# Optimization experiments

Measured on AMD Instinct MI355X. Metric: run time of the kernel, lower is better.

The kernel has to match this reference:

```python
import jax, jax.numpy as jnp
import numpy as np

EMB = 512
HEADS = 8


def setup_inputs() -> dict:
    key = jax.random.key(0)
    ks = jax.random.split(key, 5)
    B, N, E = 4, 2048, EMB
    x = jax.random.normal(ks[0], (B, N, E), dtype=jnp.float32)
    # Linear weights stored [in, out] so y = x @ W + b (matches torch x @ W.T + b with W.T)
    W_qkv = jax.random.normal(ks[1], (E, 3 * E), dtype=jnp.float32) * (E ** -0.5)
    b_qkv = jax.random.normal(ks[2], (3 * E,), dtype=jnp.float32) * 0.02
    W_proj = jax.random.normal(ks[3], (E, E), dtype=jnp.float32) * (E ** -0.5)
    b_proj = jax.random.normal(ks[4], (E,), dtype=jnp.float32) * 0.02
    return {"x": x, "W_qkv": W_qkv, "b_qkv": b_qkv, "W_proj": W_proj, "b_proj": b_proj}


def reference(x, W_qkv, b_qkv, W_proj, b_proj):
    B, N, E = x.shape
    H = HEADS
    D = E // H
    qkv = x @ W_qkv + b_qkv                      # [B, N, 3E]
    # einops 'b n (h d qkv) -> qkv b h n d': last dim splits as (h, d, 3) -> q/k/v interleaved
    qkv = qkv.reshape(B, N, H, D, 3)
    q = jnp.transpose(qkv[..., 0], (0, 2, 1, 3))  # [B, H, N, D]
    k = jnp.transpose(qkv[..., 1], (0, 2, 1, 3))
    v = jnp.transpose(qkv[..., 2], (0, 2, 1, 3))
    scale = jnp.asarray(E, x.dtype) ** 0.5        # divides by sqrt(emb_size), as in source
    energies = jnp.einsum('bhqd,bhkd->bhqk', q, k) / scale
    attention = jax.nn.softmax(energies, axis=-1)
    out = jnp.einsum('bhqk,bhkd->bhqd', attention, v)
    out = jnp.transpose(out, (0, 2, 1, 3)).reshape(B, N, E)
    return out @ W_proj + b_proj
```

## Files before the change

### kernel.cpp

```cpp
#include <hip/hip_runtime.h>
#include <hip/hip_bf16.h>

typedef __hip_bfloat16 bf16;
typedef __attribute__((ext_vector_type(8))) short short8;
typedef __attribute__((ext_vector_type(4))) float f32x4;
typedef __attribute__((ext_vector_type(16))) float f32x16;

static constexpr float QSCALE = 1.4426950408889634f / 22.627416997969522f;

__device__ __forceinline__ void gload_lds16(const void* g, void* l) {
  __builtin_amdgcn_global_load_lds((const __attribute__((address_space(1))) unsigned*)(g),
                                   (__attribute__((address_space(3))) unsigned*)(l), 16, 0, 0);
}

__device__ __forceinline__ unsigned cvtpk(float a, float b) {
  unsigned r;
  asm("v_cvt_pk_bf16_f32 %0, %1, %2" : "=v"(r) : "v"(a), "v"(b));
  return r;
}

__global__ __launch_bounds__(256) void cvt_x_kernel(const float* __restrict__ x,
                                                    bf16* __restrict__ xb, int n8) {
  for (int i = blockIdx.x * 256 + threadIdx.x; i < n8; i += gridDim.x * 256) {
    const float4* src = (const float4*)(x) + (size_t)i * 2;
    float4 a = src[0], b = src[1];
    union { short8 v; unsigned u[4]; } o;
    o.u[0] = cvtpk(a.x, a.y);
    o.u[1] = cvtpk(a.z, a.w);
    o.u[2] = cvtpk(b.x, b.y);
    o.u[3] = cvtpk(b.z, b.w);
    *(short8*)(xb + (size_t)i * 8) = o.v;
  }
}

__global__ __launch_bounds__(256) void transpose_cvt(const float* __restrict__ W,
                                                     bf16* __restrict__ Wt,
                                                     int Nout, int permute) {
  __shared__ float tile[64][65];
  const int j0 = blockIdx.x * 64, k0 = blockIdx.y * 64;
  const int tx = threadIdx.x & 63, ty = threadIdx.x >> 6;
  for (int r = ty; r < 64; r += 4)
    tile[r][tx] = W[(size_t)(k0 + r) * Nout + j0 + tx];
  __syncthreads();
  for (int r = ty; r < 64; r += 4) {
    int j = j0 + r;
    int jp = j;
    if (permute) {
      int h = j / 192, rr = j % 192, d = rr / 3, s = rr % 3;
      jp = s * 512 + h * 64 + d;
    }
    Wt[(size_t)jp * 512 + k0 + tx] = __float2bfloat16(tile[tx][r]);
  }
}

template <int MODE>
__global__ __launch_bounds__(256) void gemm_bt(const bf16* __restrict__ A,
                                               const bf16* __restrict__ Bt,
                                               const float* __restrict__ bias,
                                               bf16* __restrict__ Qb, bf16* __restrict__ Kb,
                                               bf16* __restrict__ Vt,
                                               float* __restrict__ Cout) {
  __shared__ short Alds[128 * 32];
  __shared__ short Blds[128 * 32];
  const int t = threadIdx.x;
  const int w = t >> 6;
  const int wr = w >> 1, wc = w & 1;
  const int lr = t & 15;
  const int lq = (t >> 4) & 3;
  const int bm = blockIdx.x, bn = blockIdx.y;

  f32x4 acc[4][4];
#pragma unroll
  for (int m = 0; m < 4; ++m)
#pragma unroll
    for (int n = 0; n < 4; ++n)
#pragma unroll
      for (int j = 0; j < 4; ++j) acc[m][n][j] = 0.f;

  for (int kt = 0; kt < 16; ++kt) {
#pragma unroll
    for (int i = 0; i < 2; ++i) {
      const int c = i * 256 + t;
      gload_lds16(A + (size_t)(bm * 128 + (c >> 2)) * 512 + kt * 32 + (c & 3) * 8,
                  &Alds[(i * 256 + w * 64) * 8]);
      gload_lds16(Bt + (size_t)(bn * 128 + (c >> 2)) * 512 + kt * 32 + (c & 3) * 8,
                  &Blds[(i * 256 + w * 64) * 8]);
    }
    __syncthreads();
    short8 af[4], bfr[4];
#pragma unroll
    for (int m = 0; m < 4; ++m)
      af[m] = *(const short8*)&Alds[(wr * 64 + m * 16 + lr) * 32 + lq * 8];
#pragma unroll
    for (int n = 0; n < 4; ++n)
      bfr[n] = *(const short8*)&Blds[(wc * 64 + n * 16 + lr) * 32 + lq * 8];
#pragma unroll
    for (int m = 0; m < 4; ++m)
#pragma unroll
      for (int n = 0; n < 4; ++n)
        acc[m][n] = __builtin_amdgcn_mfma_f32_16x16x32_bf16(af[m], bfr[n], acc[m][n], 0, 0, 0);
    __syncthreads();
  }

#pragma unroll
  for (int m = 0; m < 4; ++m) {
#pragma unroll
    for (int n = 0; n < 4; ++n) {
      const int col = bn * 128 + wc * 64 + n * 16 + lr;
#pragma unroll
      for (int j = 0; j < 4; ++j) {
        const int row = bm * 128 + wr * 64 + m * 16 + lq * 4 + j;
        float v = acc[m][n][j];
        if (MODE == 0) {
          const int s = col >> 9, h = (col >> 6) & 7, d = col & 63;
          v += bias[h * 192 + d * 3 + s];
          const int hd = col & 511;
          if (s == 0)
            Qb[(size_t)row * 512 + hd] = __float2bfloat16(v * QSCALE);
          else if (s == 1)
            Kb[(size_t)row * 512 + hd] = __float2bfloat16(v);
          else
            Vt[((size_t)((row >> 11) * 8 + h) * 64 + d) * 2048 + (row & 2047)] =
                __float2bfloat16(v);
        } else {
          v += bias[col];
          Cout[(size_t)row * 512 + col] = v;
        }
      }
    }
  }
}

__global__ __launch_bounds__(128) void attn_fwd(const bf16* __restrict__ Q,
                                                const bf16* __restrict__ K,
                                                const bf16* __restrict__ Vt,
                                                bf16* __restrict__ O) {
  __shared__ short Klds[2][64 * 64];
  __shared__ short Vlds[2][64 * 64];
  const int t = threadIdx.x;
  const int w = t >> 6;
  const int l = t & 63;
  const int lo = l & 31;
  const int hi = l >> 5;
  const int bid = blockIdx.x;
  const int bh = bid & 31, qt = bid >> 5;
  const int b = bh >> 3, h = bh & 7;
  const int qg = qt * 64 + w * 32 + lo;

  const bf16* Kb = K + (size_t)b * 2048 * 512 + h * 64;
  const bf16* Vb = Vt + (size_t)bh * 64 * 2048;

  const bf16* qptr = Q + ((size_t)b * 2048 + qg) * 512 + h * 64 + hi * 8;
  short8 qf[4];
#pragma unroll
  for (int kk = 0; kk < 4; ++kk) qf[kk] = *(const short8*)(qptr + kk * 16);

  union { unsigned u[4]; short8 v; } ones;
#pragma unroll
  for (int j = 0; j < 4; ++j) ones.u[j] = 0x3F803F80u;

  f32x16 zv;
#pragma unroll
  for (int r = 0; r < 16; ++r) zv[r] = 0.f;

  f32x16 acc0, acc1, ssum;
#pragma unroll
  for (int r = 0; r < 16; ++r) { acc0[r] = 0.f; acc1[r] = 0.f; ssum[r] = 0.f; }

#define STAGE(BUF, KV0)                                                              \
  do {                                                                               \
    _Pragma("unroll") for (int i = 0; i < 4; ++i) {                                  \
      const int c = i * 128 + t, r = c >> 3, g = (c & 7) ^ (r & 7);                  \
      gload_lds16(Kb + (size_t)((KV0) + r) * 512 + g * 8,                            \
                  &Klds[BUF][(i * 128 + w * 64) * 8]);                               \
    }                                                                                \
    _Pragma("unroll") for (int i = 0; i < 4; ++i) {                                  \
      const int c = i * 128 + t, r = c >> 3, g = (c & 7) ^ (r & 7);                  \
      gload_lds16(Vb + (size_t)r * 2048 + (KV0) + g * 8,                             \
                  &Vlds[BUF][(i * 128 + w * 64) * 8]);                               \
    }                                                                                \
  } while (0)

  STAGE(0, 0);
  __syncthreads();

  int buf = 0;
  for (int it = 0; it < 32; ++it) {
    if (it + 1 < 32) STAGE(buf ^ 1, (it + 1) * 64);

    const char* kl = (const char*)&Klds[buf][0];
    const char* vl = (const char*)&Vlds[buf][0];

    f32x16 s0, s1;
    __builtin_amdgcn_s_setprio(1);
#pragma unroll
    for (int kk = 0; kk < 4; ++kk) {
      short8 kf0 = *(const short8*)(kl + (lo << 7) + ((((kk << 1) | hi) ^ (lo & 7)) << 4));
      short8 kf1 = *(const short8*)(kl + ((32 + lo) << 7) + ((((kk << 1) | hi) ^ (lo & 7)) << 4));
      s0 = __builtin_amdgcn_mfma_f32_32x32x16_bf16(kf0, qf[kk], kk ? s0 : zv, 0, 0, 0);
      s1 = __builtin_amdgcn_mfma_f32_32x32x16_bf16(kf1, qf[kk], kk ? s1 : zv, 0, 0, 0);
    }
    __builtin_amdgcn_s_setprio(0);

    short8 vf[2][4];
#pragma unroll
    for (int dt = 0; dt < 2; ++dt)
#pragma unroll
      for (int ks = 0; ks < 4; ++ks)
        vf[dt][ks] = *(const short8*)(vl + ((dt * 32 + lo) << 7) +
                                      ((((ks << 1) | hi) ^ (lo & 7)) << 4));

#pragma unroll
    for (int r = 0; r < 16; ++r) s0[r] = __builtin_amdgcn_exp2f(s0[r]);
#pragma unroll
    for (int r = 0; r < 16; ++r) s1[r] = __builtin_amdgcn_exp2f(s1[r]);

    short8 pb[4];
#pragma unroll
    for (int grp = 0; grp < 4; ++grp) {
      const int ks = grp & 1;
      float p0, p1, p2, p3, p4, p5, p6, p7;
      if (grp < 2) {
        p0 = s0[8 * ks + 0]; p1 = s0[8 * ks + 1]; p2 = s0[8 * ks + 2]; p3 = s0[8 * ks + 3];
        p4 = s0[8 * ks + 4]; p5 = s0[8 * ks + 5]; p6 = s0[8 * ks + 6]; p7 = s0[8 * ks + 7];
      } else {
        p0 = s1[8 * ks + 0]; p1 = s1[8 * ks + 1]; p2 = s1[8 * ks + 2]; p3 = s1[8 * ks + 3];
        p4 = s1[8 * ks + 4]; p5 = s1[8 * ks + 5]; p6 = s1[8 * ks + 6]; p7 = s1[8 * ks + 7];
      }
      unsigned a0 = cvtpk(p0, p1);
      unsigned a1 = cvtpk(p2, p3);
      unsigned b0 = cvtpk(p4, p5);
      unsigned b1 = cvtpk(p6, p7);
      asm("v_permlane32_swap_b32 %0, %1" : "+v"(a0), "+v"(b0));
      asm("v_permlane32_swap_b32 %0, %1" : "+v"(a1), "+v"(b1));
      union { unsigned u[4]; short8 v; } pu;
      pu.u[0] = a0; pu.u[1] = a1; pu.u[2] = b0; pu.u[3] = b1;
      pb[grp] = pu.v;
    }

    __builtin_amdgcn_s_setprio(1);
#pragma unroll
    for (int ks = 0; ks < 4; ++ks) {
      acc0 = __builtin_amdgcn_mfma_f32_32x32x16_bf16(vf[0][ks], pb[ks], acc0, 0, 0, 0);
      acc1 = __builtin_amdgcn_mfma_f32_32x32x16_bf16(vf[1][ks], pb[ks], acc1, 0, 0, 0);
      ssum = __builtin_amdgcn_mfma_f32_32x32x16_bf16(ones.v, pb[ks], ssum, 0, 0, 0);
    }
    __builtin_amdgcn_s_setprio(0);

    __syncthreads();
    buf ^= 1;
  }
#undef STAGE

  const float rl = 1.0f / ssum[0];
  bf16* op = O + ((size_t)b * 2048 + qg) * 512 + h * 64;
#pragma unroll
  for (int r = 0; r < 16; ++r) {
    const int d = (r & 3) + 8 * (r >> 2) + 4 * hi;
    op[d] = __float2bfloat16(acc0[r] * rl);
    op[32 + d] = __float2bfloat16(acc1[r] * rl);
  }
}

extern "C" void kernel_launch(void* const* d_in, const int* in_sizes, int n_in,
                              void* d_out, int out_size, void* d_ws, size_t ws_size,
                              hipStream_t stream) {
  const float* x = (const float*)d_in[0];
  const float* Wqkv = (const float*)d_in[1];
  const float* bqkv = (const float*)d_in[2];
  const float* Wproj = (const float*)d_in[3];
  const float* bproj = (const float*)d_in[4];
  float* out = (float*)d_out;

  char* ws = (char*)d_ws;
  bf16* xb = (bf16*)ws;
  bf16* Wqkvt = xb + (size_t)8192 * 512;
  bf16* Wprojt = Wqkvt + (size_t)1536 * 512;
  bf16* Qb = Wprojt + (size_t)512 * 512;
  bf16* Kb = Qb + (size_t)8192 * 512;
  bf16* Vt = Kb + (size_t)8192 * 512;
  bf16* Ob = xb;

  cvt_x_kernel<<<2048, 256, 0, stream>>>(x, xb, 8192 * 512 / 8);
  transpose_cvt<<<dim3(24, 8), 256, 0, stream>>>(Wqkv, Wqkvt, 1536, 1);
  transpose_cvt<<<dim3(8, 8), 256, 0, stream>>>(Wproj, Wprojt, 512, 0);
  gemm_bt<0><<<dim3(64, 12), 256, 0, stream>>>(xb, Wqkvt, bqkv, Qb, Kb, Vt, nullptr);
  attn_fwd<<<1024, 128, 0, stream>>>(Qb, Kb, Vt, Ob);
  gemm_bt<1><<<dim3(64, 4), 256, 0, stream>>>(Ob, Wprojt, bproj, nullptr, nullptr, nullptr, out);
}
```

Baseline: 111.6 us.

## Process two query tiles per wave and compute row sums with VALU adds

Each wave now handles 64 query rows as two 32-row sub-tiles, so every K/V fragment loaded from LDS feeds twice as many MFMAs, and the grid halves to 512 blocks. The softmax denominator is no longer computed by an extra MFMA against a ones vector. It is accumulated with scalar adds of the exponentials and combined across half-waves with a shuffle. This costs more registers for the doubled accumulators and query fragments, and there are fewer blocks to fill the CUs.

```diff
diff --git a/kernel.cpp b/kernel.cpp
--- a/kernel.cpp
+++ b/kernel.cpp
@@ -145,27 +145,27 @@
   const int bid = blockIdx.x;
   const int bh = bid & 31, qt = bid >> 5;
   const int b = bh >> 3, h = bh & 7;
-  const int qg = qt * 64 + w * 32 + lo;
+  const int qgA = qt * 128 + w * 64 + lo;
 
   const bf16* Kb = K + (size_t)b * 2048 * 512 + h * 64;
   const bf16* Vb = Vt + (size_t)bh * 64 * 2048;
 
-  const bf16* qptr = Q + ((size_t)b * 2048 + qg) * 512 + h * 64 + hi * 8;
-  short8 qf[4];
-#pragma unroll
-  for (int kk = 0; kk < 4; ++kk) qf[kk] = *(const short8*)(qptr + kk * 16);
-
-  union { unsigned u[4]; short8 v; } ones;
-#pragma unroll
-  for (int j = 0; j < 4; ++j) ones.u[j] = 0x3F803F80u;
+  const bf16* qptrA = Q + ((size_t)b * 2048 + qgA) * 512 + h * 64 + hi * 8;
+  short8 qfA[4], qfB[4];
+#pragma unroll
+  for (int kk = 0; kk < 4; ++kk) {
+    qfA[kk] = *(const short8*)(qptrA + kk * 16);
+    qfB[kk] = *(const short8*)(qptrA + 32 * 512 + kk * 16);
+  }
 
   f32x16 zv;
 #pragma unroll
   for (int r = 0; r < 16; ++r) zv[r] = 0.f;
 
-  f32x16 acc0, acc1, ssum;
-#pragma unroll
-  for (int r = 0; r < 16; ++r) { acc0[r] = 0.f; acc1[r] = 0.f; ssum[r] = 0.f; }
+  f32x16 accA0, accA1, accB0, accB1;
+#pragma unroll
+  for (int r = 0; r < 16; ++r) { accA0[r] = 0.f; accA1[r] = 0.f; accB0[r] = 0.f; accB1[r] = 0.f; }
+  float lsA = 0.f, lsB = 0.f;
 
 #define STAGE(BUF, KV0)                                                              \
   do {                                                                               \
@@ -184,81 +184,102 @@
   STAGE(0, 0);
   __syncthreads();
 
-  int buf = 0;
+#pragma unroll 2
   for (int it = 0; it < 32; ++it) {
+    const int buf = it & 1;
     if (it + 1 < 32) STAGE(buf ^ 1, (it + 1) * 64);
 
     const char* kl = (const char*)&Klds[buf][0];
     const char* vl = (const char*)&Vlds[buf][0];
 
-    f32x16 s0, s1;
-    __builtin_amdgcn_s_setprio(1);
-#pragma unroll
-    for (int kk = 0; kk < 4; ++kk) {
-      short8 kf0 = *(const short8*)(kl + (lo << 7) + ((((kk << 1) | hi) ^ (lo & 7)) << 4));
-      short8 kf1 = *(const short8*)(kl + ((32 + lo) << 7) + ((((kk << 1) | hi) ^ (lo & 7)) << 4));
-      s0 = __builtin_amdgcn_mfma_f32_32x32x16_bf16(kf0, qf[kk], kk ? s0 : zv, 0, 0, 0);
-      s1 = __builtin_amdgcn_mfma_f32_32x32x16_bf16(kf1, qf[kk], kk ? s1 : zv, 0, 0, 0);
+#pragma unroll
+    for (int sh = 0; sh < 2; ++sh) {
+      short8 kf[4];
+#pragma unroll
+      for (int kk = 0; kk < 4; ++kk)
+        kf[kk] = *(const short8*)(kl + ((sh * 32 + lo) << 7) +
+                                  ((((kk << 1) | hi) ^ (lo & 7)) << 4));
+
+      f32x16 sA, sB;
+      __builtin_amdgcn_s_setprio(1);
+#pragma unroll
+      for (int kk = 0; kk < 4; ++kk) {
+        sA = __builtin_amdgcn_mfma_f32_32x32x16_bf16(kf[kk], qfA[kk], kk ? sA : zv, 0, 0, 0);
+        sB = __builtin_amdgcn_mfma_f32_32x32x16_bf16(kf[kk], qfB[kk], kk ? sB : zv, 0, 0, 0);
+      }
+      __builtin_amdgcn_s_setprio(0);
+
+      short8 vf[2][2];
+#pragma unroll
+      for (int dt = 0; dt < 2; ++dt)
+#pragma unroll
+        for (int j = 0; j < 2; ++j)
+          vf[dt][j] = *(const short8*)(vl + ((dt * 32 + lo) << 7) +
+                                       (((((sh * 2 + j) << 1) | hi) ^ (lo & 7)) << 4));
+
+      float tA = 0.f, tB = 0.f;
+#pragma unroll
+      for (int r = 0; r < 16; ++r) { sA[r] = __builtin_amdgcn_exp2f(sA[r]); tA += sA[r]; }
+#pragma unroll
+      for (int r = 0; r < 16; ++r) { sB[r] = __builtin_amdgcn_exp2f(sB[r]); tB += sB[r]; }
+      lsA += tA;
+      lsB += tB;
+
+      short8 pbA[2], pbB[2];
+#pragma unroll
+      for (int g = 0; g < 2; ++g) {
+        {
+          unsigned a0 = cvtpk(sA[8 * g + 0], sA[8 * g + 1]);
+          unsigned a1 = cvtpk(sA[8 * g + 2], sA[8 * g + 3]);
+          unsigned b0 = cvtpk(sA[8 * g + 4], sA[8 * g + 5]);
+          unsigned b1 = cvtpk(sA[8 * g + 6], sA[8 * g + 7]);
+          asm("v_permlane32_swap_b32 %0, %1" : "+v"(a0), "+v"(b0));
+          asm("v_permlane32_swap_b32 %0, %1" : "+v"(a1), "+v"(b1));
+          union { unsigned u[4]; short8 v; } pu;
+          pu.u[0] = a0; pu.u[1] = a1; pu.u[2] = b0; pu.u[3] = b1;
+          pbA[g] = pu.v;
+        }
+        {
+          unsigned a0 = cvtpk(sB[8 * g + 0], sB[8 * g + 1]);
+          unsigned a1 = cvtpk(sB[8 * g + 2], sB[8 * g + 3]);
+          unsigned b0 = cvtpk(sB[8 * g + 4], sB[8 * g + 5]);
+          unsigned b1 = cvtpk(sB[8 * g + 6], sB[8 * g + 7]);
+          asm("v_permlane32_swap_b32 %0, %1" : "+v"(a0), "+v"(b0));
+          asm("v_permlane32_swap_b32 %0, %1" : "+v"(a1), "+v"(b1));
+          union { unsigned u[4]; short8 v; } pu;
+          pu.u[0] = a0; pu.u[1] = a1; pu.u[2] = b0; pu.u[3] = b1;
+          pbB[g] = pu.v;
+        }
+      }
+
+      __builtin_amdgcn_s_setprio(1);
+#pragma unroll
+      for (int j = 0; j < 2; ++j) {
+        accA0 = __builtin_amdgcn_mfma_f32_32x32x16_bf16(vf[0][j], pbA[j], accA0, 0, 0, 0);
+        accA1 = __builtin_amdgcn_mfma_f32_32x32x16_bf16(vf[1][j], pbA[j], accA1, 0, 0, 0);
+        accB0 = __builtin_amdgcn_mfma_f32_32x32x16_bf16(vf[0][j], pbB[j], accB0, 0, 0, 0);
+        accB1 = __builtin_amdgcn_mfma_f32_32x32x16_bf16(vf[1][j], pbB[j], accB1, 0, 0, 0);
+      }
+      __builtin_amdgcn_s_setprio(0);
     }
-    __builtin_amdgcn_s_setprio(0);
-
-    short8 vf[2][4];
-#pragma unroll
-    for (int dt = 0; dt < 2; ++dt)
-#pragma unroll
-      for (int ks = 0; ks < 4; ++ks)
-        vf[dt][ks] = *(const short8*)(vl + ((dt * 32 + lo) << 7) +
-                                      ((((ks << 1) | hi) ^ (lo & 7)) << 4));
-
-#pragma unroll
-    for (int r = 0; r < 16; ++r) s0[r] = __builtin_amdgcn_exp2f(s0[r]);
-#pragma unroll
-    for (int r = 0; r < 16; ++r) s1[r] = __builtin_amdgcn_exp2f(s1[r]);
-
-    short8 pb[4];
-#pragma unroll
-    for (int grp = 0; grp < 4; ++grp) {
-      const int ks = grp & 1;
-      float p0, p1, p2, p3, p4, p5, p6, p7;
-      if (grp < 2) {
-        p0 = s0[8 * ks + 0]; p1 = s0[8 * ks + 1]; p2 = s0[8 * ks + 2]; p3 = s0[8 * ks + 3];
-        p4 = s0[8 * ks + 4]; p5 = s0[8 * ks + 5]; p6 = s0[8 * ks + 6]; p7 = s0[8 * ks + 7];
-      } else {
-        p0 = s1[8 * ks + 0]; p1 = s1[8 * ks + 1]; p2 = s1[8 * ks + 2]; p3 = s1[8 * ks + 3];
-        p4 = s1[8 * ks + 4]; p5 = s1[8 * ks + 5]; p6 = s1[8 * ks + 6]; p7 = s1[8 * ks + 7];
-      }
-      unsigned a0 = cvtpk(p0, p1);
-      unsigned a1 = cvtpk(p2, p3);
-      unsigned b0 = cvtpk(p4, p5);
-      unsigned b1 = cvtpk(p6, p7);
-      asm("v_permlane32_swap_b32 %0, %1" : "+v"(a0), "+v"(b0));
-      asm("v_permlane32_swap_b32 %0, %1" : "+v"(a1), "+v"(b1));
-      union { unsigned u[4]; short8 v; } pu;
-      pu.u[0] = a0; pu.u[1] = a1; pu.u[2] = b0; pu.u[3] = b1;
-      pb[grp] = pu.v;
-    }
-
-    __builtin_amdgcn_s_setprio(1);
-#pragma unroll
-    for (int ks = 0; ks < 4; ++ks) {
-      acc0 = __builtin_amdgcn_mfma_f32_32x32x16_bf16(vf[0][ks], pb[ks], acc0, 0, 0, 0);
-      acc1 = __builtin_amdgcn_mfma_f32_32x32x16_bf16(vf[1][ks], pb[ks], acc1, 0, 0, 0);
-      ssum = __builtin_amdgcn_mfma_f32_32x32x16_bf16(ones.v, pb[ks], ssum, 0, 0, 0);
-    }
-    __builtin_amdgcn_s_setprio(0);
 
     __syncthreads();
-    buf ^= 1;
   }
 #undef STAGE
 
-  const float rl = 1.0f / ssum[0];
-  bf16* op = O + ((size_t)b * 2048 + qg) * 512 + h * 64;
+  lsA += __shfl_xor(lsA, 32);
+  lsB += __shfl_xor(lsB, 32);
+  const float rlA = 1.0f / lsA;
+  const float rlB = 1.0f / lsB;
+  bf16* opA = O + ((size_t)b * 2048 + qgA) * 512 + h * 64;
+  bf16* opB = opA + 32 * 512;
 #pragma unroll
   for (int r = 0; r < 16; ++r) {
     const int d = (r & 3) + 8 * (r >> 2) + 4 * hi;
-    op[d] = __float2bfloat16(acc0[r] * rl);
-    op[32 + d] = __float2bfloat16(acc1[r] * rl);
+    opA[d] = __float2bfloat16(accA0[r] * rlA);
+    opA[32 + d] = __float2bfloat16(accA1[r] * rlA);
+    opB[d] = __float2bfloat16(accB0[r] * rlB);
+    opB[32 + d] = __float2bfloat16(accB1[r] * rlB);
   }
 }
 
@@ -285,6 +306,6 @@
   transpose_cvt<<<dim3(24, 8), 256, 0, stream>>>(Wqkv, Wqkvt, 1536, 1);
   transpose_cvt<<<dim3(8, 8), 256, 0, stream>>>(Wproj, Wprojt, 512, 0);
   gemm_bt<0><<<dim3(64, 12), 256, 0, stream>>>(xb, Wqkvt, bqkv, Qb, Kb, Vt, nullptr);
-  attn_fwd<<<1024, 128, 0, stream>>>(Qb, Kb, Vt, Ob);
+  attn_fwd<<<512, 128, 0, stream>>>(Qb, Kb, Vt, Ob);
   gemm_bt<1><<<dim3(64, 4), 256, 0, stream>>>(Ob, Wprojt, bproj, nullptr, nullptr, nullptr, out);
 }
```

Result: faster. 106.9 us (-4.2%).
